# Kernel tuning notes

Hardware: AMD Instinct MI355X
Metric: run time of the kernel (lower is better)

The kernel has to match this reference:

```python
import jax, jax.numpy as jnp
import numpy as np

K, N, D = 128, 512, 256
THETA = 784.0
BATCH = 16384


def _expm_np(M):
    # scaling-and-squaring Taylor expm in float64 numpy (deterministic, no scipy)
    nrm = np.linalg.norm(M, 1)
    s = max(0, int(np.ceil(np.log2(max(nrm, 1.0)))) + 1)
    A = M / (2.0 ** s)
    E = np.eye(M.shape[0])
    term = np.eye(M.shape[0])
    for i in range(1, 30):
        term = term @ A / i
        E = E + term
    for _ in range(s):
        E = E @ E
    return E


def _legendre_zoh(theta, order):
    Q = np.arange(order, dtype=np.float64)
    R = (2 * Q + 1)[:, None] / theta
    j, i = np.meshgrid(Q, Q)
    A = np.where(i < j, -1.0, (-1.0) ** (i - j + 1)) * R
    B = (-1.0) ** Q[:, None] * R
    # ZOH discretization with dt=1: expm([[A, B], [0, 0]])
    M = np.zeros((order + 1, order + 1))
    M[:order, :order] = A
    M[:order, order:] = B
    E = _expm_np(M)
    return E[:order, :order], E[:order, order:]  # Ad (d,d), Bd (d,1)


def setup_inputs() -> dict:
    key = jax.random.key(0)
    ks = jax.random.split(key, 9)
    x = jax.random.normal(ks[0], (BATCH, K), dtype=jnp.float32)
    h = jax.random.normal(ks[1], (BATCH, N), dtype=jnp.float32)
    m = jax.random.normal(ks[2], (BATCH, D), dtype=jnp.float32)
    # xavier-normal-ish weights
    Wx = jax.random.normal(ks[3], (N, K), dtype=jnp.float32) * np.sqrt(2.0 / (N + K))
    Wh = jax.random.normal(ks[4], (N, N), dtype=jnp.float32) * np.sqrt(2.0 / (N + N))
    Wm = jax.random.normal(ks[5], (N, D), dtype=jnp.float32) * np.sqrt(2.0 / (N + D))
    lim = np.sqrt(3.0 / D)
    ex = jax.random.uniform(ks[6], (1, K), dtype=jnp.float32, minval=-lim, maxval=lim)
    eh = jax.random.uniform(ks[7], (1, N), dtype=jnp.float32, minval=-lim, maxval=lim)
    em = jnp.zeros((1, D), dtype=jnp.float32)
    Ad, Bd = _legendre_zoh(THETA, D)
    AT = jnp.asarray(Ad, dtype=jnp.float32)  # (d, d)
    BT = jnp.asarray(Bd, dtype=jnp.float32)  # (d, 1)
    return {"x": x, "h": h, "m": m, "Wx": Wx, "Wh": Wh, "Wm": Wm,
            "ex": ex, "eh": eh, "em": em, "AT": AT, "BT": BT}


def reference(x, h, m, Wx, Wh, Wm, ex, eh, em, AT, BT):
    # u: (B, 1) scalar input signal per batch element
    u = x @ ex.T + h @ eh.T + m @ em.T
    # memory update: m' = m A^T + u B^T  -> (B, d)
    new_m = m @ AT.T + u @ BT.T
    # hidden update: h' = sigmoid(x Wx^T + h Wh^T + m' Wm^T)
    new_h = jax.nn.sigmoid(x @ Wx.T + h @ Wh.T + new_m @ Wm.T)
    return (new_h, new_m)
```

## Files before the change

### kernel.cpp

```cpp
#include <hip/hip_runtime.h>


typedef __bf16 bf16;
typedef bf16  bf16x8 __attribute__((ext_vector_type(8)));
typedef bf16  bf16x4 __attribute__((ext_vector_type(4)));
typedef float f32x4  __attribute__((ext_vector_type(4)));
typedef unsigned short u16;

#define BATCH 16384
#define BM 32
#define WPACK_OFF 0
#define ATPACK_OFF 458752
#define PACK_TOTAL 524288

#define XS 0
#define HS 8192
#define MS 40960
#define UL 57344
#define SMEM_BYTES 57472

__device__ __forceinline__ u16 f2bf(float f) {
  unsigned u = __builtin_bit_cast(unsigned, f);
  u += 0x7FFFu + ((u >> 16) & 1u);
  return (u16)(u >> 16);
}

__device__ __forceinline__ int swz(int row, int cb) {
  return cb ^ ((row & 7) << 4);
}

__global__ __launch_bounds__(256) void lmu_pack(
    const float* __restrict__ Wx, const float* __restrict__ Wh,
    const float* __restrict__ Wm, const float* __restrict__ AT,
    u16* __restrict__ ws) {
  int i = blockIdx.x * 256 + threadIdx.x;
  if (i < 458752) {
    int j = i & 7, rest = i >> 3;
    int n = rest & 511, kk = rest >> 9;
    int k = kk * 8 + j;
    float v = (k < 128) ? Wx[n * 128 + k]
            : (k < 640) ? Wh[n * 512 + (k - 128)]
                        : Wm[n * 256 + (k - 640)];
    ws[WPACK_OFF + i] = f2bf(v);
  } else if (i < PACK_TOTAL) {
    int t = i - 458752;
    int j = t & 7, rest = t >> 3;
    int d = rest & 255, kk = rest >> 8;
    ws[i] = f2bf(AT[d * 256 + kk * 8 + j]);
  }
}

__global__ __launch_bounds__(512, 4) void lmu_fused(
    const float* __restrict__ x, const float* __restrict__ h,
    const float* __restrict__ m, const float* __restrict__ ex,
    const float* __restrict__ eh, const float* __restrict__ em,
    const float* __restrict__ BT, const u16* __restrict__ ws,
    float* __restrict__ out) {
  __shared__ __align__(16) char smem[SMEM_BYTES];
  const int tid  = threadIdx.x;
  const int lane = tid & 63;
  const int w    = tid >> 6;
  const int lm   = lane & 15;
  const int kg   = lane >> 4;
  const int b0   = blockIdx.x * BM;

  const u16* wpack  = ws + WPACK_OFF;
  const u16* atpack = ws + ATPACK_OFF;

  {
    const float4* xg = (const float4*)(x + (size_t)b0 * 128);
#pragma unroll
    for (int it = 0; it < 2; ++it) {
      int f = it * 512 + tid;
      int r = f >> 5, c4 = f & 31;
      float4 v = xg[f];
      bf16x4 b = {(bf16)v.x, (bf16)v.y, (bf16)v.z, (bf16)v.w};
      *(bf16x4*)(smem + XS + r * 256 + swz(r, c4 * 8)) = b;
    }
    const float4* hg = (const float4*)(h + (size_t)b0 * 512);
#pragma unroll
    for (int it = 0; it < 8; ++it) {
      int f = it * 512 + tid;
      int r = f >> 7, c4 = f & 127;
      float4 v = hg[f];
      bf16x4 b = {(bf16)v.x, (bf16)v.y, (bf16)v.z, (bf16)v.w};
      *(bf16x4*)(smem + HS + r * 1024 + swz(r, c4 * 8)) = b;
    }
    const float4* mg = (const float4*)(m + (size_t)b0 * 256);
#pragma unroll
    for (int it = 0; it < 4; ++it) {
      int f = it * 512 + tid;
      int r = f >> 6, c4 = f & 63;
      float4 v = mg[f];
      bf16x4 b = {(bf16)v.x, (bf16)v.y, (bf16)v.z, (bf16)v.w};
      *(bf16x4*)(smem + MS + r * 512 + swz(r, c4 * 8)) = b;
    }
  }
  __syncthreads();

  {
    const int row = tid >> 4;
    const int q   = tid & 15;
    float s = 0.f;
#pragma unroll
    for (int j = 0; j < 7; ++j) {
      int k = q * 56 + j * 8;
      int base, rowb, klocal;
      const float* ep;
      if (k < 128)      { base = XS; rowb = 256;  klocal = k;       ep = ex + k; }
      else if (k < 640) { base = HS; rowb = 1024; klocal = k - 128; ep = eh + (k - 128); }
      else              { base = MS; rowb = 512;  klocal = k - 640; ep = em + (k - 640); }
      bf16x8 a = *(const bf16x8*)(smem + base + row * rowb + swz(row, klocal * 2));
      float4 e0 = *(const float4*)ep;
      float4 e1 = *(const float4*)(ep + 4);
      s += (float)a[0] * e0.x + (float)a[1] * e0.y + (float)a[2] * e0.z + (float)a[3] * e0.w;
      s += (float)a[4] * e1.x + (float)a[5] * e1.y + (float)a[6] * e1.z + (float)a[7] * e1.w;
    }
    s += __shfl_xor(s, 1);
    s += __shfl_xor(s, 2);
    s += __shfl_xor(s, 4);
    s += __shfl_xor(s, 8);
    if (q == 0) ((float*)(smem + UL))[row] = s;
  }
  __syncthreads();

  {
    const float* u = (const float*)(smem + UL);
    const int c0 = w * 32 + lm;
    float bt0 = BT[c0], bt1 = BT[c0 + 16];
    f32x4 accm[2][2];
#pragma unroll
    for (int mt = 0; mt < 2; ++mt)
#pragma unroll
      for (int r2 = 0; r2 < 4; ++r2) {
        float uv = u[mt * 16 + kg * 4 + r2];
        accm[mt][0][r2] = uv * bt0;
        accm[mt][1][r2] = uv * bt1;
      }
#pragma unroll
    for (int ks = 0; ks < 8; ++ks) {
      bf16x8 a[2];
#pragma unroll
      for (int mt = 0; mt < 2; ++mt) {
        int row = mt * 16 + lm;
        a[mt] = *(const bf16x8*)(smem + MS + row * 512 + swz(row, (ks * 32 + kg * 8) * 2));
      }
#pragma unroll
      for (int ct = 0; ct < 2; ++ct) {
        bf16x8 b = *(const bf16x8*)(atpack + (((ks * 4 + kg) * 256) + c0 + ct * 16) * 8);
#pragma unroll
        for (int mt = 0; mt < 2; ++mt)
          accm[mt][ct] = __builtin_amdgcn_mfma_f32_16x16x32_bf16(a[mt], b, accm[mt][ct], 0, 0, 0);
      }
    }
    float* outm = out + (size_t)BATCH * 512;
#pragma unroll
    for (int mt = 0; mt < 2; ++mt)
#pragma unroll
      for (int r2 = 0; r2 < 4; ++r2) {
        size_t row = (size_t)(b0 + mt * 16 + kg * 4 + r2);
        outm[row * 256 + c0]      = accm[mt][0][r2];
        outm[row * 256 + c0 + 16] = accm[mt][1][r2];
      }
    __syncthreads();
#pragma unroll
    for (int mt = 0; mt < 2; ++mt)
#pragma unroll
      for (int r2 = 0; r2 < 4; ++r2) {
        int rr = mt * 16 + kg * 4 + r2;
        *(bf16*)(smem + MS + rr * 512 + swz(rr, c0 * 2))        = (bf16)accm[mt][0][r2];
        *(bf16*)(smem + MS + rr * 512 + swz(rr, (c0 + 16) * 2)) = (bf16)accm[mt][1][r2];
      }
  }
  __syncthreads();

  {
    f32x4 acc[2][4];
    const f32x4 vzero = {0.f, 0.f, 0.f, 0.f};
#pragma unroll
    for (int mt = 0; mt < 2; ++mt)
#pragma unroll
      for (int ct = 0; ct < 4; ++ct) acc[mt][ct] = vzero;
    const int cb = w * 64 + lm;

    auto step = [&](int base, int rowb, int klocal, int kkg) {
      bf16x8 a[2];
#pragma unroll
      for (int mt = 0; mt < 2; ++mt) {
        int row = mt * 16 + lm;
        a[mt] = *(const bf16x8*)(smem + base + row * rowb + swz(row, (klocal + kg * 8) * 2));
      }
#pragma unroll
      for (int ct = 0; ct < 4; ++ct) {
        bf16x8 b = *(const bf16x8*)(wpack + (((kkg + kg) * 512) + cb + ct * 16) * 8);
#pragma unroll
        for (int mt = 0; mt < 2; ++mt)
          acc[mt][ct] = __builtin_amdgcn_mfma_f32_16x16x32_bf16(a[mt], b, acc[mt][ct], 0, 0, 0);
      }
    };
#pragma unroll
    for (int ks = 0; ks < 4; ++ks)  step(XS, 256,  ks * 32, ks * 4);
#pragma unroll
    for (int ks = 0; ks < 16; ++ks) step(HS, 1024, ks * 32, 16 + ks * 4);
#pragma unroll
    for (int ks = 0; ks < 8; ++ks)  step(MS, 512,  ks * 32, 80 + ks * 4);

#pragma unroll
    for (int mt = 0; mt < 2; ++mt)
#pragma unroll
      for (int r2 = 0; r2 < 4; ++r2) {
        size_t row = (size_t)(b0 + mt * 16 + kg * 4 + r2);
#pragma unroll
        for (int ct = 0; ct < 4; ++ct) {
          float v = acc[mt][ct][r2];
          out[row * 512 + cb + ct * 16] = 1.0f / (1.0f + __expf(-v));
        }
      }
  }
}

extern "C" void kernel_launch(void* const* d_in, const int* in_sizes, int n_in,
                              void* d_out, int out_size, void* d_ws, size_t ws_size,
                              hipStream_t stream) {
  const float* x  = (const float*)d_in[0];
  const float* h  = (const float*)d_in[1];
  const float* m  = (const float*)d_in[2];
  const float* Wx = (const float*)d_in[3];
  const float* Wh = (const float*)d_in[4];
  const float* Wm = (const float*)d_in[5];
  const float* ex = (const float*)d_in[6];
  const float* eh = (const float*)d_in[7];
  const float* em = (const float*)d_in[8];
  const float* AT = (const float*)d_in[9];
  const float* BT = (const float*)d_in[10];
  float* out = (float*)d_out;
  u16* ws = (u16*)d_ws;

  lmu_pack<<<PACK_TOTAL / 256, 256, 0, stream>>>(Wx, Wh, Wm, AT, ws);
  lmu_fused<<<BATCH / BM, 512, 0, stream>>>(x, h, m, ex, eh, em, BT, ws, out);
}
```

Before: 64.23 us.

## Fold memory update into hidden GEMM via precomputed Wm·A and Wm·B

Precomputes Wm·A^T and Wm·B in fp32 setup kernels, so the hidden pre-activation becomes a single GEMM over the original m (plus a rank-1 u term). The m' result no longer has to be finished and round-tripped through shared memory before the hidden GEMM. The fused kernel now processes 64 rows per block, streams x/h/m in 128-wide K chunks through double-buffered shared memory while the global loads overlap the MFMA work, and computes u on the fly. It adds an extra setup kernel and changes numerics slightly, since m' is no longer rounded to bf16 before multiplying by Wm. It also lowers occupancy because of the larger accumulator set.

```diff
diff --git a/kernel.cpp b/kernel.cpp
--- a/kernel.cpp
+++ b/kernel.cpp
@@ -3,28 +3,21 @@
 
 typedef __bf16 bf16;
 typedef bf16  bf16x8 __attribute__((ext_vector_type(8)));
-typedef bf16  bf16x4 __attribute__((ext_vector_type(4)));
 typedef float f32x4  __attribute__((ext_vector_type(4)));
 typedef unsigned short u16;
 
 #define BATCH 16384
-#define BM 32
-#define WPACK_OFF 0
-#define ATPACK_OFF 458752
-#define PACK_TOTAL 524288
-
-#define XS 0
-#define HS 8192
-#define MS 40960
-#define UL 57344
-#define SMEM_BYTES 57472
+#define BM 64
+#define WPACK 0
+#define ATPACK 458752
+#define WUOFF 524288
+#define PACK_ITEMS 393728
 
 __device__ __forceinline__ u16 f2bf(float f) {
   unsigned u = __builtin_bit_cast(unsigned, f);
   u += 0x7FFFu + ((u >> 16) & 1u);
   return (u16)(u >> 16);
 }
-
 __device__ __forceinline__ int swz(int row, int cb) {
   return cb ^ ((row & 7) << 4);
 }
@@ -32,191 +25,188 @@
 __global__ __launch_bounds__(256) void lmu_pack(
     const float* __restrict__ Wx, const float* __restrict__ Wh,
     const float* __restrict__ Wm, const float* __restrict__ AT,
-    u16* __restrict__ ws) {
+    const float* __restrict__ BT, u16* __restrict__ ws) {
   int i = blockIdx.x * 256 + threadIdx.x;
-  if (i < 458752) {
+  if (i < 327680) {
     int j = i & 7, rest = i >> 3;
     int n = rest & 511, kk = rest >> 9;
     int k = kk * 8 + j;
-    float v = (k < 128) ? Wx[n * 128 + k]
-            : (k < 640) ? Wh[n * 512 + (k - 128)]
-                        : Wm[n * 256 + (k - 640)];
-    ws[WPACK_OFF + i] = f2bf(v);
-  } else if (i < PACK_TOTAL) {
-    int t = i - 458752;
+    float v = (k < 128) ? Wx[n * 128 + k] : Wh[n * 512 + (k - 128)];
+    ws[WPACK + i] = f2bf(v);
+  } else if (i < 393216) {
+    int t = i - 327680;
     int j = t & 7, rest = t >> 3;
     int d = rest & 255, kk = rest >> 8;
-    ws[i] = f2bf(AT[d * 256 + kk * 8 + j]);
-  }
-}
-
-__global__ __launch_bounds__(512, 4) void lmu_fused(
+    ws[ATPACK + t] = f2bf(AT[d * 256 + kk * 8 + j]);
+  } else if (i < PACK_ITEMS) {
+    int n = i - 393216;
+    float s = 0.f;
+    for (int k = 0; k < 256; k += 4) {
+      float4 wv = *(const float4*)(Wm + (size_t)n * 256 + k);
+      float4 bv = *(const float4*)(BT + k);
+      s += wv.x * bv.x + wv.y * bv.y + wv.z * bv.z + wv.w * bv.w;
+    }
+    ((float*)(ws + WUOFF))[n] = s;
+  }
+}
+
+__global__ __launch_bounds__(256) void lmu_wm2(
+    const float* __restrict__ Wm, const float* __restrict__ AT,
+    u16* __restrict__ ws) {
+  __shared__ float wmt[16 * 256];
+  const int t = threadIdx.x;
+  const int nb = blockIdx.x * 16, db = blockIdx.y * 64;
+#pragma unroll
+  for (int it = 0; it < 4; ++it) {
+    int f = it * 256 + t;
+    float4 v = *(const float4*)(Wm + (size_t)(nb + (f >> 6)) * 256 + (f & 63) * 4);
+    *(float4*)(wmt + (f >> 6) * 256 + (f & 63) * 4) = v;
+  }
+  __syncthreads();
+  const int d = db + (t & 63);
+  const int nn = (t >> 6) * 4;
+  float acc[4] = {0.f, 0.f, 0.f, 0.f};
+  for (int k = 0; k < 256; ++k) {
+    float atv = AT[(size_t)k * 256 + d];
+#pragma unroll
+    for (int i2 = 0; i2 < 4; ++i2) acc[i2] += wmt[(nn + i2) * 256 + k] * atv;
+  }
+  const int kk = 80 + (d >> 3), j = d & 7;
+#pragma unroll
+  for (int i2 = 0; i2 < 4; ++i2)
+    ws[WPACK + ((size_t)kk * 512 + (nb + nn + i2)) * 8 + j] = f2bf(acc[i2]);
+}
+
+__global__ __launch_bounds__(512, 2) void lmu_fused(
     const float* __restrict__ x, const float* __restrict__ h,
     const float* __restrict__ m, const float* __restrict__ ex,
     const float* __restrict__ eh, const float* __restrict__ em,
     const float* __restrict__ BT, const u16* __restrict__ ws,
     float* __restrict__ out) {
-  __shared__ __align__(16) char smem[SMEM_BYTES];
+  __shared__ __align__(16) char smem[2 * 16384 + 256];
+  float* uL = (float*)(smem + 2 * 16384);
+
   const int tid  = threadIdx.x;
   const int lane = tid & 63;
   const int w    = tid >> 6;
+  const int wr   = w >> 2;
+  const int wc   = w & 3;
   const int lm   = lane & 15;
   const int kg   = lane >> 4;
   const int b0   = blockIdx.x * BM;
-
-  const u16* wpack  = ws + WPACK_OFF;
-  const u16* atpack = ws + ATPACK_OFF;
-
-  {
-    const float4* xg = (const float4*)(x + (size_t)b0 * 128);
-#pragma unroll
-    for (int it = 0; it < 2; ++it) {
-      int f = it * 512 + tid;
-      int r = f >> 5, c4 = f & 31;
-      float4 v = xg[f];
-      bf16x4 b = {(bf16)v.x, (bf16)v.y, (bf16)v.z, (bf16)v.w};
-      *(bf16x4*)(smem + XS + r * 256 + swz(r, c4 * 8)) = b;
-    }
-    const float4* hg = (const float4*)(h + (size_t)b0 * 512);
-#pragma unroll
-    for (int it = 0; it < 8; ++it) {
-      int f = it * 512 + tid;
-      int r = f >> 7, c4 = f & 127;
-      float4 v = hg[f];
-      bf16x4 b = {(bf16)v.x, (bf16)v.y, (bf16)v.z, (bf16)v.w};
-      *(bf16x4*)(smem + HS + r * 1024 + swz(r, c4 * 8)) = b;
-    }
-    const float4* mg = (const float4*)(m + (size_t)b0 * 256);
-#pragma unroll
-    for (int it = 0; it < 4; ++it) {
-      int f = it * 512 + tid;
-      int r = f >> 6, c4 = f & 63;
-      float4 v = mg[f];
-      bf16x4 b = {(bf16)v.x, (bf16)v.y, (bf16)v.z, (bf16)v.w};
-      *(bf16x4*)(smem + MS + r * 512 + swz(r, c4 * 8)) = b;
-    }
-  }
-  __syncthreads();
-
-  {
-    const int row = tid >> 4;
-    const int q   = tid & 15;
+  const int r    = tid >> 3;
+  const int k0   = (tid & 7) * 16;
+
+  const u16* wpk = ws + WPACK;
+  const u16* atp = ws + ATPACK;
+  const float* wuf = (const float*)(ws + WUOFF);
+
+  f32x4 acc[2][8];
+  f32x4 acc2[2][4];
+#pragma unroll
+  for (int mt = 0; mt < 2; ++mt) {
+#pragma unroll
+    for (int ct = 0; ct < 8; ++ct) acc[mt][ct] = (f32x4){0.f, 0.f, 0.f, 0.f};
+#pragma unroll
+    for (int ct = 0; ct < 4; ++ct) acc2[mt][ct] = (f32x4){0.f, 0.f, 0.f, 0.f};
+  }
+  float ureg = 0.f;
+  float4 av[4], ev[4];
+
+  auto stage_load = [&](int c) {
+    const float *ap, *ep;
+    if (c == 0)      { ap = x + (size_t)(b0 + r) * 128 + k0;                 ep = ex + k0; }
+    else if (c < 5)  { ap = h + (size_t)(b0 + r) * 512 + (c - 1) * 128 + k0; ep = eh + (c - 1) * 128 + k0; }
+    else             { ap = m + (size_t)(b0 + r) * 256 + (c - 5) * 128 + k0; ep = em + (c - 5) * 128 + k0; }
+#pragma unroll
+    for (int i = 0; i < 4; ++i) { av[i] = *(const float4*)(ap + i * 4); ev[i] = *(const float4*)(ep + i * 4); }
+  };
+  auto stage_commit = [&](char* bufp) {
     float s = 0.f;
 #pragma unroll
-    for (int j = 0; j < 7; ++j) {
-      int k = q * 56 + j * 8;
-      int base, rowb, klocal;
-      const float* ep;
-      if (k < 128)      { base = XS; rowb = 256;  klocal = k;       ep = ex + k; }
-      else if (k < 640) { base = HS; rowb = 1024; klocal = k - 128; ep = eh + (k - 128); }
-      else              { base = MS; rowb = 512;  klocal = k - 640; ep = em + (k - 640); }
-      bf16x8 a = *(const bf16x8*)(smem + base + row * rowb + swz(row, klocal * 2));
-      float4 e0 = *(const float4*)ep;
-      float4 e1 = *(const float4*)(ep + 4);
-      s += (float)a[0] * e0.x + (float)a[1] * e0.y + (float)a[2] * e0.z + (float)a[3] * e0.w;
-      s += (float)a[4] * e1.x + (float)a[5] * e1.y + (float)a[6] * e1.z + (float)a[7] * e1.w;
-    }
-    s += __shfl_xor(s, 1);
-    s += __shfl_xor(s, 2);
-    s += __shfl_xor(s, 4);
-    s += __shfl_xor(s, 8);
-    if (q == 0) ((float*)(smem + UL))[row] = s;
-  }
-  __syncthreads();
-
-  {
-    const float* u = (const float*)(smem + UL);
-    const int c0 = w * 32 + lm;
-    float bt0 = BT[c0], bt1 = BT[c0 + 16];
-    f32x4 accm[2][2];
-#pragma unroll
-    for (int mt = 0; mt < 2; ++mt)
-#pragma unroll
-      for (int r2 = 0; r2 < 4; ++r2) {
-        float uv = u[mt * 16 + kg * 4 + r2];
-        accm[mt][0][r2] = uv * bt0;
-        accm[mt][1][r2] = uv * bt1;
-      }
-#pragma unroll
-    for (int ks = 0; ks < 8; ++ks) {
+    for (int i = 0; i < 4; ++i)
+      s += av[i].x * ev[i].x + av[i].y * ev[i].y + av[i].z * ev[i].z + av[i].w * ev[i].w;
+    ureg += s;
+    bf16x8 p0 = {(bf16)av[0].x, (bf16)av[0].y, (bf16)av[0].z, (bf16)av[0].w,
+                 (bf16)av[1].x, (bf16)av[1].y, (bf16)av[1].z, (bf16)av[1].w};
+    bf16x8 p1 = {(bf16)av[2].x, (bf16)av[2].y, (bf16)av[2].z, (bf16)av[2].w,
+                 (bf16)av[3].x, (bf16)av[3].y, (bf16)av[3].z, (bf16)av[3].w};
+    *(bf16x8*)(bufp + r * 256 + swz(r, k0 * 2))      = p0;
+    *(bf16x8*)(bufp + r * 256 + swz(r, k0 * 2 + 16)) = p1;
+  };
+  auto mma_chunk = [&](const char* bufp, int c) {
+#pragma unroll
+    for (int ks = 0; ks < 4; ++ks) {
       bf16x8 a[2];
 #pragma unroll
       for (int mt = 0; mt < 2; ++mt) {
-        int row = mt * 16 + lm;
-        a[mt] = *(const bf16x8*)(smem + MS + row * 512 + swz(row, (ks * 32 + kg * 8) * 2));
-      }
-#pragma unroll
-      for (int ct = 0; ct < 2; ++ct) {
-        bf16x8 b = *(const bf16x8*)(atpack + (((ks * 4 + kg) * 256) + c0 + ct * 16) * 8);
-#pragma unroll
-        for (int mt = 0; mt < 2; ++mt)
-          accm[mt][ct] = __builtin_amdgcn_mfma_f32_16x16x32_bf16(a[mt], b, accm[mt][ct], 0, 0, 0);
-      }
-    }
-    float* outm = out + (size_t)BATCH * 512;
-#pragma unroll
-    for (int mt = 0; mt < 2; ++mt)
-#pragma unroll
-      for (int r2 = 0; r2 < 4; ++r2) {
-        size_t row = (size_t)(b0 + mt * 16 + kg * 4 + r2);
-        outm[row * 256 + c0]      = accm[mt][0][r2];
-        outm[row * 256 + c0 + 16] = accm[mt][1][r2];
-      }
-    __syncthreads();
-#pragma unroll
-    for (int mt = 0; mt < 2; ++mt)
-#pragma unroll
-      for (int r2 = 0; r2 < 4; ++r2) {
-        int rr = mt * 16 + kg * 4 + r2;
-        *(bf16*)(smem + MS + rr * 512 + swz(rr, c0 * 2))        = (bf16)accm[mt][0][r2];
-        *(bf16*)(smem + MS + rr * 512 + swz(rr, (c0 + 16) * 2)) = (bf16)accm[mt][1][r2];
-      }
-  }
-  __syncthreads();
-
-  {
-    f32x4 acc[2][4];
-    const f32x4 vzero = {0.f, 0.f, 0.f, 0.f};
-#pragma unroll
-    for (int mt = 0; mt < 2; ++mt)
-#pragma unroll
-      for (int ct = 0; ct < 4; ++ct) acc[mt][ct] = vzero;
-    const int cb = w * 64 + lm;
-
-    auto step = [&](int base, int rowb, int klocal, int kkg) {
-      bf16x8 a[2];
-#pragma unroll
-      for (int mt = 0; mt < 2; ++mt) {
-        int row = mt * 16 + lm;
-        a[mt] = *(const bf16x8*)(smem + base + row * rowb + swz(row, (klocal + kg * 8) * 2));
-      }
-#pragma unroll
-      for (int ct = 0; ct < 4; ++ct) {
-        bf16x8 b = *(const bf16x8*)(wpack + (((kkg + kg) * 512) + cb + ct * 16) * 8);
+        int row = wr * 32 + mt * 16 + lm;
+        a[mt] = *(const bf16x8*)(bufp + row * 256 + swz(row, (ks * 32 + kg * 8) * 2));
+      }
+      const u16* wp = wpk + ((size_t)(c * 16 + ks * 4 + kg) * 512) * 8;
+#pragma unroll
+      for (int ct = 0; ct < 8; ++ct) {
+        bf16x8 b = *(const bf16x8*)(wp + (wc * 128 + ct * 16 + lm) * 8);
 #pragma unroll
         for (int mt = 0; mt < 2; ++mt)
           acc[mt][ct] = __builtin_amdgcn_mfma_f32_16x16x32_bf16(a[mt], b, acc[mt][ct], 0, 0, 0);
       }
-    };
-#pragma unroll
-    for (int ks = 0; ks < 4; ++ks)  step(XS, 256,  ks * 32, ks * 4);
-#pragma unroll
-    for (int ks = 0; ks < 16; ++ks) step(HS, 1024, ks * 32, 16 + ks * 4);
-#pragma unroll
-    for (int ks = 0; ks < 8; ++ks)  step(MS, 512,  ks * 32, 80 + ks * 4);
-
-#pragma unroll
-    for (int mt = 0; mt < 2; ++mt)
-#pragma unroll
-      for (int r2 = 0; r2 < 4; ++r2) {
-        size_t row = (size_t)(b0 + mt * 16 + kg * 4 + r2);
+      if (c >= 5) {
+        const u16* ap2 = atp + ((size_t)((c - 5) * 16 + ks * 4 + kg) * 256) * 8;
 #pragma unroll
         for (int ct = 0; ct < 4; ++ct) {
-          float v = acc[mt][ct][r2];
-          out[row * 512 + cb + ct * 16] = 1.0f / (1.0f + __expf(-v));
+          bf16x8 b = *(const bf16x8*)(ap2 + (wc * 64 + ct * 16 + lm) * 8);
+#pragma unroll
+          for (int mt = 0; mt < 2; ++mt)
+            acc2[mt][ct] = __builtin_amdgcn_mfma_f32_16x16x32_bf16(a[mt], b, acc2[mt][ct], 0, 0, 0);
         }
       }
-  }
+    }
+  };
+
+  stage_load(0);
+  stage_commit(smem);
+  __syncthreads();
+#pragma unroll
+  for (int c = 0; c < 7; ++c) {
+    char* cur = smem + (c & 1) * 16384;
+    char* nxt = smem + ((c + 1) & 1) * 16384;
+    if (c < 6) stage_load(c + 1);
+    mma_chunk(cur, c);
+    if (c < 6) stage_commit(nxt);
+    __syncthreads();
+  }
+
+  float s = ureg;
+  s += __shfl_xor(s, 1);
+  s += __shfl_xor(s, 2);
+  s += __shfl_xor(s, 4);
+  if ((tid & 7) == 0) uL[r] = s;
+  __syncthreads();
+
+  float wuv[8];
+#pragma unroll
+  for (int ct = 0; ct < 8; ++ct) wuv[ct] = wuf[wc * 128 + ct * 16 + lm];
+  float btv[4];
+#pragma unroll
+  for (int ct = 0; ct < 4; ++ct) btv[ct] = BT[wc * 64 + ct * 16 + lm];
+  float* outm = out + (size_t)BATCH * 512;
+#pragma unroll
+  for (int mt = 0; mt < 2; ++mt)
+#pragma unroll
+    for (int j = 0; j < 4; ++j) {
+      int rl = wr * 32 + mt * 16 + kg * 4 + j;
+      float uv = uL[rl];
+      size_t grow = (size_t)(b0 + rl);
+#pragma unroll
+      for (int ct = 0; ct < 8; ++ct) {
+        float v = acc[mt][ct][j] + uv * wuv[ct];
+        out[grow * 512 + wc * 128 + ct * 16 + lm] = 1.0f / (1.0f + __expf(-v));
+      }
+#pragma unroll
+      for (int ct = 0; ct < 4; ++ct)
+        outm[grow * 256 + wc * 64 + ct * 16 + lm] = acc2[mt][ct][j] + uv * btv[ct];
+    }
 }
 
 extern "C" void kernel_launch(void* const* d_in, const int* in_sizes, int n_in,
@@ -236,6 +226,7 @@
   float* out = (float*)d_out;
   u16* ws = (u16*)d_ws;
 
-  lmu_pack<<<PACK_TOTAL / 256, 256, 0, stream>>>(Wx, Wh, Wm, AT, ws);
+  lmu_pack<<<(PACK_ITEMS + 255) / 256, 256, 0, stream>>>(Wx, Wh, Wm, AT, BT, ws);
+  lmu_wm2<<<dim3(32, 4), 256, 0, stream>>>(Wm, AT, ws);
   lmu_fused<<<BATCH / BM, 512, 0, stream>>>(x, h, m, ex, eh, em, BT, ws, out);
 }
```

Result: slower. 113.5 us (+76.6%).
